# Performance work log

Measured on AMD Instinct MI355X. Metric: run time of the kernel, lower is better.

Reference implementation:

```python
import jax, jax.numpy as jnp
import numpy as np

N, F, K, O = 8192, 512, 2, 64
FMIN = jnp.finfo(jnp.float32).min


def setup_inputs() -> dict:
    key = jax.random.key(0)
    k1, k2, k3, k4, k5 = jax.random.split(key, 5)
    H = jax.random.normal(k1, (N, F), dtype=jnp.float32)
    # sparse-ish binary adjacency with self-loops (float mask, as in TF code)
    A = (jax.random.uniform(k2, (N, N)) < 0.0125).astype(jnp.float32)
    A = jnp.maximum(A, jnp.eye(N, dtype=jnp.float32))
    idx = jnp.arange(N, dtype=jnp.int32)
    W = jax.random.normal(k3, (K, F, O), dtype=jnp.float32) * 0.1
    b = jnp.zeros((K, O), dtype=jnp.float32)
    a1 = jax.random.normal(k4, (K, O), dtype=jnp.float32) * 0.1
    a2 = jax.random.normal(k5, (K, O), dtype=jnp.float32) * 0.1
    return {"H": H, "A": A, "idx": idx, "W": W, "b": b, "a1": a1, "a2": a2}


def reference(H, A, idx, W, b, a1, a2):
    # batch_A = tf.gather(A, idx, axis=1)
    batch_A = A[:, idx]                                  # [N, N]
    HW = jnp.einsum('nf,kfo->kno', H, W)                 # [K, N, O]
    attn1 = jnp.einsum('kno,ko->kn', HW, a1)             # [K, N]
    attn2 = jnp.einsum('kno,ko->kn', HW, a2)             # [K, N]
    # transpose(meshgrid sum): scores[k, i, j] = attn1[k, i] + attn2[k, j]
    scores = attn1[:, :, None] + attn2[:, None, :]       # [K, N, N]
    scores = scores + FMIN * (1.0 - batch_A)[None]
    scores = jnp.where(scores >= 0, scores, 0.2 * scores)  # LeakyReLU(0.2)
    attn = jax.nn.softmax(scores, axis=-1)               # [K, N, N]
    # res = transpose(HW^T @ attn) => res[k, i] = sum_j attn[k, j, i] * HW[k, j]
    res = jnp.einsum('kji,kjo->kio', attn, HW)           # [K, N, O]
    out = jax.nn.relu(res + b[:, None, :])               # [K, N, O]
    # concat heads along feature axis
    return jnp.transpose(out, (1, 0, 2)).reshape(N, K * O)
```

## Files before the change

### kernel.cpp

```cpp
#include <hip/hip_runtime.h>

#define NN 8192
#define FD 512
typedef unsigned long long u64;

__device__ __forceinline__ unsigned f2bf(float x) {
  unsigned u = __float_as_uint(x);
  u += 0x7FFFu + ((u >> 16) & 1u);
  return u >> 16;
}

__device__ __forceinline__ int flt2key(float f) {
  int i = __float_as_int(f);
  return i >= 0 ? i : (i ^ 0x7FFFFFFF);
}
__device__ __forceinline__ float key2flt(int k) {
  return __int_as_float(k >= 0 ? k : (k ^ 0x7FFFFFFF));
}

__device__ __forceinline__ int col0_of_word(int w) {
  return ((w >> 5) << 11) + (((w >> 2) & 7) << 8) + (w & 3);
}

__global__ __launch_bounds__(256) void k1_hw(
    const float* __restrict__ H, const float* __restrict__ W,
    const float* __restrict__ a1, const float* __restrict__ a2,
    const int* __restrict__ idx, int* __restrict__ flag,
    unsigned short* __restrict__ hw2, float* __restrict__ c1, float* __restrict__ c2p,
    int* __restrict__ gkey) {
  if (blockIdx.x >= 512) {
    const int t = (blockIdx.x - 512) * 256 + threadIdx.x;
    int4 v = ((const int4*)idx)[t];
    const int base = t * 4;
    bool bad = (v.x != base) | (v.y != base + 1) | (v.z != base + 2) | (v.w != base + 3);
    const bool any = (__ballot(bad) != 0ULL);
    if ((threadIdx.x & 63) == 0) atomicMax(flag, any ? 1 : 0);
    return;
  }
  const int k    = blockIdx.x & 1;
  const int wv   = threadIdx.x >> 6;
  const int lane = threadIdx.x & 63;
  const int nbase = __builtin_amdgcn_readfirstlane((blockIdx.x >> 1) * 32 + wv * 8);
  const float* __restrict__ Wk = W + k * (FD * 64);
  float acc[8] = {0.f,0.f,0.f,0.f,0.f,0.f,0.f,0.f};
  for (int f = 0; f < FD; f += 4) {
    float w0 = Wk[(f+0)*64 + lane];
    float w1 = Wk[(f+1)*64 + lane];
    float w2 = Wk[(f+2)*64 + lane];
    float w3 = Wk[(f+3)*64 + lane];
#pragma unroll
    for (int r = 0; r < 8; ++r) {
      float4 h = *(const float4*)(H + (size_t)(nbase + r) * FD + f);
      acc[r] = fmaf(h.x, w0, acc[r]);
      acc[r] = fmaf(h.y, w1, acc[r]);
      acc[r] = fmaf(h.z, w2, acc[r]);
      acc[r] = fmaf(h.w, w3, acc[r]);
    }
  }
  const float a1v = a1[k*64 + lane];
  const float a2v = a2[k*64 + lane];
  float wmax = -3.4e38f;
#pragma unroll
  for (int r = 0; r < 8; ++r) {
    const int n = nbase + r;
    hw2[((size_t)n * 64 + lane) * 2 + k] = (unsigned short)f2bf(acc[r]);
    float t1 = acc[r] * a1v;
    float t2 = acc[r] * a2v;
#pragma unroll
    for (int off = 32; off; off >>= 1) {
      t1 += __shfl_down(t1, off);
      t2 += __shfl_down(t2, off);
    }
    if (lane == 0) {
      c1[k*NN + n] = t1;
      c2p[n*2 + k] = t2;
      wmax = fmaxf(wmax, t2);
    }
  }
  if (lane == 0) atomicMax(&gkey[k], flt2key(wmax));
}

__global__ __launch_bounds__(256) void k2_scan(
    const float* __restrict__ A, const int* __restrict__ idx, const int* __restrict__ flag,
    const int* __restrict__ gkey,
    const float* __restrict__ c1, const float* __restrict__ c2p,
    u64* __restrict__ mask, float4* __restrict__ param2) {
  __shared__ u64 sm[128];
  __shared__ float redl[2][4];
  const int tid = threadIdx.x;
  const int wv = tid >> 6, lane = tid & 63;
  const int j = blockIdx.x;
  const bool fast = (flag[0] == 0);
  const float* __restrict__ Arow = A + (size_t)j * NN;

  float4 a[8];
  if (fast) {
#pragma unroll
    for (int p = 0; p < 8; ++p)
      a[p] = *(const float4*)(Arow + wv * 2048 + p * 256 + lane * 4);
  } else {
#pragma unroll
    for (int p = 0; p < 8; ++p) {
      const int c0 = wv * 2048 + p * 256 + lane * 4;
      a[p].x = Arow[idx[c0+0]]; a[p].y = Arow[idx[c0+1]];
      a[p].z = Arow[idx[c0+2]]; a[p].w = Arow[idx[c0+3]];
    }
  }
#pragma unroll
  for (int p = 0; p < 8; ++p) {
    const float av[4] = {a[p].x, a[p].y, a[p].z, a[p].w};
#pragma unroll
    for (int c = 0; c < 4; ++c) {
      const u64 bal = __ballot(av[c] != 0.f);
      if (lane == 0) sm[wv * 32 + p * 4 + c] = bal;
    }
  }
  __syncthreads();
  if (tid < 64) {
    ulonglong2 v;
    v.x = sm[tid * 2];
    v.y = sm[tid * 2 + 1];
    *(ulonglong2*)(mask + (size_t)j * 128 + tid * 2) = v;
  }
  const float c10 = c1[j];
  const float c11 = c1[NN + j];
  float M0 = c10 + key2flt(gkey[0]); M0 = (M0 >= 0.f) ? M0 : 0.2f * M0;
  float M1 = c11 + key2flt(gkey[1]); M1 = (M1 >= 0.f) ? M1 : 0.2f * M1;
  float s0 = 0.f, s1 = 0.f;
  if (tid < 128) {
    u64 m = sm[tid];
    const int cb = col0_of_word(tid);
    while (m) {
      const int b = __builtin_ctzll(m);
      m &= m - 1;
      const float2 cv = *(const float2*)(c2p + (cb + 4 * b) * 2);
      float v0 = c10 + cv.x; v0 = (v0 >= 0.f) ? v0 : 0.2f * v0;
      s0 += __expf(v0 - M0);
      float v1 = c11 + cv.y; v1 = (v1 >= 0.f) ? v1 : 0.2f * v1;
      s1 += __expf(v1 - M1);
    }
  }
#pragma unroll
  for (int off = 32; off; off >>= 1) {
    s0 += __shfl_down(s0, off);
    s1 += __shfl_down(s1, off);
  }
  if (lane == 0) { redl[0][wv] = s0; redl[1][wv] = s1; }
  __syncthreads();
  if (tid == 0) {
    float S0 = redl[0][0] + redl[0][1] + redl[0][2] + redl[0][3];
    float S1 = redl[1][0] + redl[1][1] + redl[1][2] + redl[1][3];
    const float I0 = (S0 > 0.f) ? 1.f / S0 : 0.f;
    const float I1 = (S1 > 0.f) ? 1.f / S1 : 0.f;
    param2[j*2 + 0] = make_float4(c10, (S0 > 0.f) ? M0 : 0.f, I0, 0.f);
    param2[j*2 + 1] = make_float4(c11, (S1 > 0.f) ? M1 : 0.f, I1, 0.f);
  }
}

__device__ __forceinline__ u64 xpose64(u64 x, int lane) {
  const u64 M[6] = {0x00000000FFFFFFFFULL, 0x0000FFFF0000FFFFULL,
                    0x00FF00FF00FF00FFULL, 0x0F0F0F0F0F0F0F0FULL,
                    0x3333333333333333ULL, 0x5555555555555555ULL};
  int d = 32;
#pragma unroll
  for (int s = 0; s < 6; ++s, d >>= 1) {
    u64 y = __shfl_xor(x, d);
    const u64 ML = M[s], MH = ~ML;
    if ((lane & d) == 0) x = (x & ML) | ((y & ML) << d);
    else                 x = (x & MH) | ((y & MH) >> d);
  }
  return x;
}

__global__ __launch_bounds__(256) void kT(
    const u64* __restrict__ mask, unsigned short* __restrict__ edges16,
    int* __restrict__ ecnt4) {
  __shared__ unsigned short seg[4][33][64];
  __shared__ int scnt[4][64];
  const int wv = threadIdx.x >> 6, lane = threadIdx.x & 63;
  const int w  = blockIdx.x;
  const int qq = blockIdx.y;
  const int jst = qq * 2048 + wv * 512;
  int cnt = 0;
#pragma unroll 1
  for (int jt = 0; jt < 8; jt += 4) {
    u64 x[4];
#pragma unroll
    for (int t = 0; t < 4; ++t)
      x[t] = mask[(size_t)(jst + (jt + t) * 64 + lane) * 128 + w];
#pragma unroll
    for (int t = 0; t < 4; ++t) x[t] = xpose64(x[t], lane);
#pragma unroll
    for (int t = 0; t < 4; ++t) {
      u64 m = x[t];
      const int jb = jst + (jt + t) * 64;
      while (m) {
        const int r = __builtin_ctzll(m);
        m &= m - 1;
        if (cnt < 32) seg[wv][cnt][lane] = (unsigned short)(jb + r);
        ++cnt;
      }
    }
  }
  scnt[wv][lane] = min(cnt, 32);
  __syncthreads();
  for (int rr = 0; rr < 16; ++rr) {
    const int r = wv * 16 + rr;
    const int i = col0_of_word(w) + 4 * r;
    const int c0 = scnt[0][r], c1 = scnt[1][r], c2 = scnt[2][r], c3 = scnt[3][r];
    const int o1 = c0, o2 = o1 + c1, o3 = o2 + c2;
    const int tot = min(o3 + c3, 64);
    const int pos = lane;
    if (pos < tot) {
      int s, off;
      if (pos < o1)      { s = 0; off = pos; }
      else if (pos < o2) { s = 1; off = pos - o1; }
      else if (pos < o3) { s = 2; off = pos - o2; }
      else               { s = 3; off = pos - o3; }
      edges16[(size_t)i * 256 + qq * 64 + pos] = seg[s][off][r];
    }
    if (lane == 0) ecnt4[i * 4 + qq] = tot;
  }
}

__global__ __launch_bounds__(256) void k3_aggregate(
    const int* __restrict__ ecnt4, const unsigned short* __restrict__ edges16,
    const float4* __restrict__ param2, const float* __restrict__ c2p,
    const unsigned* __restrict__ hw2, const float* __restrict__ b,
    float* __restrict__ out) {
  __shared__ unsigned short ebuf[4][256];
  const int wv = threadIdx.x >> 6, lane = threadIdx.x & 63;
  const int i = __builtin_amdgcn_readfirstlane(blockIdx.x * 4 + wv);
  const float c20 = c2p[i*2];
  const float c21 = c2p[i*2 + 1];
  const int4 ec = *(const int4*)(ecnt4 + i * 4);
  const unsigned short* __restrict__ e16 = edges16 + (size_t)i * 256;
  int off = 0;
  {
    if (lane < ec.x) ebuf[wv][off + lane] = e16[lane];            off += ec.x;
    if (lane < ec.y) ebuf[wv][off + lane] = e16[64 + lane];       off += ec.y;
    if (lane < ec.z) ebuf[wv][off + lane] = e16[128 + lane];      off += ec.z;
    if (lane < ec.w) ebuf[wv][off + lane] = e16[192 + lane];      off += ec.w;
  }
  __syncthreads();
  const int cnt = off;
  float acc0 = 0.f, acc1 = 0.f;
  int t = 0;
  for (; t + 8 <= cnt; t += 8) {
    const ushort4 j1 = *(const ushort4*)(&ebuf[wv][t]);
    const ushort4 j2 = *(const ushort4*)(&ebuf[wv][t + 4]);
    const int jj[8] = {j1.x, j1.y, j1.z, j1.w, j2.x, j2.y, j2.z, j2.w};
    float4 p0[8], p1[8];
    unsigned uu[8];
#pragma unroll
    for (int s = 0; s < 8; ++s) {
      p0[s] = param2[jj[s]*2];
      p1[s] = param2[jj[s]*2 + 1];
      uu[s] = hw2[(size_t)jj[s] * 64 + lane];
    }
#pragma unroll
    for (int s = 0; s < 8; ++s) {
      float v, w;
      v = p0[s].x + c20; v = (v >= 0.f) ? v : 0.2f*v; w = __expf(v - p0[s].y) * p0[s].z;
      acc0 = fmaf(w, __uint_as_float(uu[s] << 16), acc0);
      v = p1[s].x + c21; v = (v >= 0.f) ? v : 0.2f*v; w = __expf(v - p1[s].y) * p1[s].z;
      acc1 = fmaf(w, __uint_as_float(uu[s] & 0xFFFF0000u), acc1);
    }
  }
  for (; t < cnt; ++t) {
    const int j = ebuf[wv][t];
    const float4 p0 = param2[j*2], p1 = param2[j*2+1];
    const unsigned u = hw2[(size_t)j * 64 + lane];
    float v0 = p0.x + c20; v0 = (v0 >= 0.f) ? v0 : 0.2f*v0;
    float w0 = __expf(v0 - p0.y) * p0.z;
    float v1 = p1.x + c21; v1 = (v1 >= 0.f) ? v1 : 0.2f*v1;
    float w1 = __expf(v1 - p1.y) * p1.z;
    acc0 = fmaf(w0, __uint_as_float(u << 16), acc0);
    acc1 = fmaf(w1, __uint_as_float(u & 0xFFFF0000u), acc1);
  }
  out[(size_t)i * 128 + lane]      = fmaxf(acc0 + b[lane], 0.f);
  out[(size_t)i * 128 + 64 + lane] = fmaxf(acc1 + b[64 + lane], 0.f);
}

extern "C" void kernel_launch(void* const* d_in, const int* in_sizes, int n_in,
                              void* d_out, int out_size, void* d_ws, size_t ws_size,
                              hipStream_t stream) {
  const float* H   = (const float*)d_in[0];
  const float* A   = (const float*)d_in[1];
  const int*   idx = (const int*)d_in[2];
  const float* W   = (const float*)d_in[3];
  const float* b   = (const float*)d_in[4];
  const float* a1  = (const float*)d_in[5];
  const float* a2  = (const float*)d_in[6];
  float* out = (float*)d_out;

  char* ws = (char*)d_ws;
  unsigned short* hw2     = (unsigned short*)(ws + 0);
  float*          c1      = (float*)(ws + 2097152);
  float*          c2p     = (float*)(ws + 2162688);
  float4*         param2  = (float4*)(ws + 2228224);
  int*            flag    = (int*)(ws + 2490368);
  int*            gkey    = (int*)(ws + 2490372);
  u64*            mask    = (u64*)(ws + 2490624);
  unsigned short* edges16 = (unsigned short*)(ws + 10879232);
  int*            ecnt4   = (int*)(ws + 15073536);

  k1_hw<<<520, 256, 0, stream>>>(H, W, a1, a2, idx, flag, hw2, c1, c2p, gkey);
  k2_scan<<<NN, 256, 0, stream>>>(A, idx, flag, gkey, c1, c2p, mask, param2);
  kT<<<dim3(128, 4), 256, 0, stream>>>(mask, edges16, ecnt4);
  k3_aggregate<<<NN / 4, 256, 0, stream>>>(ecnt4, edges16, param2, c2p, (const unsigned*)hw2, b, out);
}
```

Baseline: 536.2 us.

## Fuse scan, transpose and aggregate kernels into one cooperative persistent kernel

Replaces the three separate launches (row scan of A, mask transpose, aggregation) with one cooperative kernel of 512 blocks. Each block loops over 16 rows in the scan phase, then does the transpose and aggregation work, with grid-wide syncs between phases. This removes launch gaps and tail effects between kernels. In exchange it adds grid barrier overhead and lowers parallelism in the A scan, which streams 256MB from memory with only 512 blocks; occupancy is limited by launch_bounds(256,2) and the larger combined shared memory.

After: 696.6 us. 1.3x slower.

```diff
diff --git a/kernel.cpp b/kernel.cpp
--- a/kernel.cpp
+++ b/kernel.cpp
@@ -1,4 +1,7 @@
 #include <hip/hip_runtime.h>
+#include <hip/hip_cooperative_groups.h>
+
+namespace cg = cooperative_groups;
 
 #define NN 8192
 #define FD 512
@@ -80,83 +83,6 @@
   if (lane == 0) atomicMax(&gkey[k], flt2key(wmax));
 }
 
-__global__ __launch_bounds__(256) void k2_scan(
-    const float* __restrict__ A, const int* __restrict__ idx, const int* __restrict__ flag,
-    const int* __restrict__ gkey,
-    const float* __restrict__ c1, const float* __restrict__ c2p,
-    u64* __restrict__ mask, float4* __restrict__ param2) {
-  __shared__ u64 sm[128];
-  __shared__ float redl[2][4];
-  const int tid = threadIdx.x;
-  const int wv = tid >> 6, lane = tid & 63;
-  const int j = blockIdx.x;
-  const bool fast = (flag[0] == 0);
-  const float* __restrict__ Arow = A + (size_t)j * NN;
-
-  float4 a[8];
-  if (fast) {
-#pragma unroll
-    for (int p = 0; p < 8; ++p)
-      a[p] = *(const float4*)(Arow + wv * 2048 + p * 256 + lane * 4);
-  } else {
-#pragma unroll
-    for (int p = 0; p < 8; ++p) {
-      const int c0 = wv * 2048 + p * 256 + lane * 4;
-      a[p].x = Arow[idx[c0+0]]; a[p].y = Arow[idx[c0+1]];
-      a[p].z = Arow[idx[c0+2]]; a[p].w = Arow[idx[c0+3]];
-    }
-  }
-#pragma unroll
-  for (int p = 0; p < 8; ++p) {
-    const float av[4] = {a[p].x, a[p].y, a[p].z, a[p].w};
-#pragma unroll
-    for (int c = 0; c < 4; ++c) {
-      const u64 bal = __ballot(av[c] != 0.f);
-      if (lane == 0) sm[wv * 32 + p * 4 + c] = bal;
-    }
-  }
-  __syncthreads();
-  if (tid < 64) {
-    ulonglong2 v;
-    v.x = sm[tid * 2];
-    v.y = sm[tid * 2 + 1];
-    *(ulonglong2*)(mask + (size_t)j * 128 + tid * 2) = v;
-  }
-  const float c10 = c1[j];
-  const float c11 = c1[NN + j];
-  float M0 = c10 + key2flt(gkey[0]); M0 = (M0 >= 0.f) ? M0 : 0.2f * M0;
-  float M1 = c11 + key2flt(gkey[1]); M1 = (M1 >= 0.f) ? M1 : 0.2f * M1;
-  float s0 = 0.f, s1 = 0.f;
-  if (tid < 128) {
-    u64 m = sm[tid];
-    const int cb = col0_of_word(tid);
-    while (m) {
-      const int b = __builtin_ctzll(m);
-      m &= m - 1;
-      const float2 cv = *(const float2*)(c2p + (cb + 4 * b) * 2);
-      float v0 = c10 + cv.x; v0 = (v0 >= 0.f) ? v0 : 0.2f * v0;
-      s0 += __expf(v0 - M0);
-      float v1 = c11 + cv.y; v1 = (v1 >= 0.f) ? v1 : 0.2f * v1;
-      s1 += __expf(v1 - M1);
-    }
-  }
-#pragma unroll
-  for (int off = 32; off; off >>= 1) {
-    s0 += __shfl_down(s0, off);
-    s1 += __shfl_down(s1, off);
-  }
-  if (lane == 0) { redl[0][wv] = s0; redl[1][wv] = s1; }
-  __syncthreads();
-  if (tid == 0) {
-    float S0 = redl[0][0] + redl[0][1] + redl[0][2] + redl[0][3];
-    float S1 = redl[1][0] + redl[1][1] + redl[1][2] + redl[1][3];
-    const float I0 = (S0 > 0.f) ? 1.f / S0 : 0.f;
-    const float I1 = (S1 > 0.f) ? 1.f / S1 : 0.f;
-    param2[j*2 + 0] = make_float4(c10, (S0 > 0.f) ? M0 : 0.f, I0, 0.f);
-    param2[j*2 + 1] = make_float4(c11, (S1 > 0.f) ? M1 : 0.f, I1, 0.f);
-  }
-}
-
 __device__ __forceinline__ u64 xpose64(u64 x, int lane) {
   const u64 M[6] = {0x00000000FFFFFFFFULL, 0x0000FFFF0000FFFFULL,
                     0x00FF00FF00FF00FFULL, 0x0F0F0F0F0F0F0F0FULL,
@@ -172,114 +98,198 @@
   return x;
 }
 
-__global__ __launch_bounds__(256) void kT(
-    const u64* __restrict__ mask, unsigned short* __restrict__ edges16,
-    int* __restrict__ ecnt4) {
+__global__ __launch_bounds__(256, 2) void mega(
+    const float* __restrict__ A, const int* __restrict__ idx,
+    const int* __restrict__ flag, const int* __restrict__ gkey,
+    const float* __restrict__ c1, const float* __restrict__ c2p,
+    u64* __restrict__ mask, float4* __restrict__ param2,
+    unsigned short* __restrict__ edges16, int* __restrict__ ecnt4,
+    const unsigned* __restrict__ hw2, const float* __restrict__ b,
+    float* __restrict__ out) {
+  cg::grid_group grid = cg::this_grid();
+  __shared__ u64 sm[128];
+  __shared__ float redl[2][4];
   __shared__ unsigned short seg[4][33][64];
   __shared__ int scnt[4][64];
-  const int wv = threadIdx.x >> 6, lane = threadIdx.x & 63;
-  const int w  = blockIdx.x;
-  const int qq = blockIdx.y;
-  const int jst = qq * 2048 + wv * 512;
-  int cnt = 0;
+  __shared__ unsigned short ebuf[4][256];
+
+  const int tid = threadIdx.x;
+  const int wv = tid >> 6, lane = tid & 63;
+
+  {
+    const bool fast = (flag[0] == 0);
+    const float G0 = key2flt(gkey[0]);
+    const float G1 = key2flt(gkey[1]);
 #pragma unroll 1
-  for (int jt = 0; jt < 8; jt += 4) {
-    u64 x[4];
-#pragma unroll
-    for (int t = 0; t < 4; ++t)
-      x[t] = mask[(size_t)(jst + (jt + t) * 64 + lane) * 128 + w];
-#pragma unroll
-    for (int t = 0; t < 4; ++t) x[t] = xpose64(x[t], lane);
-#pragma unroll
-    for (int t = 0; t < 4; ++t) {
-      u64 m = x[t];
-      const int jb = jst + (jt + t) * 64;
-      while (m) {
-        const int r = __builtin_ctzll(m);
-        m &= m - 1;
-        if (cnt < 32) seg[wv][cnt][lane] = (unsigned short)(jb + r);
-        ++cnt;
-      }
-    }
-  }
-  scnt[wv][lane] = min(cnt, 32);
-  __syncthreads();
-  for (int rr = 0; rr < 16; ++rr) {
-    const int r = wv * 16 + rr;
-    const int i = col0_of_word(w) + 4 * r;
-    const int c0 = scnt[0][r], c1 = scnt[1][r], c2 = scnt[2][r], c3 = scnt[3][r];
-    const int o1 = c0, o2 = o1 + c1, o3 = o2 + c2;
-    const int tot = min(o3 + c3, 64);
-    const int pos = lane;
-    if (pos < tot) {
-      int s, off;
-      if (pos < o1)      { s = 0; off = pos; }
-      else if (pos < o2) { s = 1; off = pos - o1; }
-      else if (pos < o3) { s = 2; off = pos - o2; }
-      else               { s = 3; off = pos - o3; }
-      edges16[(size_t)i * 256 + qq * 64 + pos] = seg[s][off][r];
-    }
-    if (lane == 0) ecnt4[i * 4 + qq] = tot;
-  }
-}
-
-__global__ __launch_bounds__(256) void k3_aggregate(
-    const int* __restrict__ ecnt4, const unsigned short* __restrict__ edges16,
-    const float4* __restrict__ param2, const float* __restrict__ c2p,
-    const unsigned* __restrict__ hw2, const float* __restrict__ b,
-    float* __restrict__ out) {
-  __shared__ unsigned short ebuf[4][256];
-  const int wv = threadIdx.x >> 6, lane = threadIdx.x & 63;
-  const int i = __builtin_amdgcn_readfirstlane(blockIdx.x * 4 + wv);
-  const float c20 = c2p[i*2];
-  const float c21 = c2p[i*2 + 1];
-  const int4 ec = *(const int4*)(ecnt4 + i * 4);
-  const unsigned short* __restrict__ e16 = edges16 + (size_t)i * 256;
-  int off = 0;
+    for (int r = 0; r < 16; ++r) {
+      const int j = blockIdx.x * 16 + r;
+      const float* __restrict__ Arow = A + (size_t)j * NN;
+      float4 a[8];
+      if (fast) {
+#pragma unroll
+        for (int p = 0; p < 8; ++p)
+          a[p] = *(const float4*)(Arow + wv * 2048 + p * 256 + lane * 4);
+      } else {
+#pragma unroll
+        for (int p = 0; p < 8; ++p) {
+          const int c0 = wv * 2048 + p * 256 + lane * 4;
+          a[p].x = Arow[idx[c0+0]]; a[p].y = Arow[idx[c0+1]];
+          a[p].z = Arow[idx[c0+2]]; a[p].w = Arow[idx[c0+3]];
+        }
+      }
+#pragma unroll
+      for (int p = 0; p < 8; ++p) {
+        const float av[4] = {a[p].x, a[p].y, a[p].z, a[p].w};
+#pragma unroll
+        for (int c = 0; c < 4; ++c) {
+          const u64 bal = __ballot(av[c] != 0.f);
+          if (lane == 0) sm[wv * 32 + p * 4 + c] = bal;
+        }
+      }
+      __syncthreads();
+      if (tid < 64) {
+        ulonglong2 v;
+        v.x = sm[tid * 2];
+        v.y = sm[tid * 2 + 1];
+        *(ulonglong2*)(mask + (size_t)j * 128 + tid * 2) = v;
+      }
+      const float c10 = c1[j];
+      const float c11 = c1[NN + j];
+      float M0 = c10 + G0; M0 = (M0 >= 0.f) ? M0 : 0.2f * M0;
+      float M1 = c11 + G1; M1 = (M1 >= 0.f) ? M1 : 0.2f * M1;
+      float s0 = 0.f, s1 = 0.f;
+      if (tid < 128) {
+        u64 m = sm[tid];
+        const int cb = col0_of_word(tid);
+        while (m) {
+          const int bb = __builtin_ctzll(m);
+          m &= m - 1;
+          const float2 cv = *(const float2*)(c2p + (cb + 4 * bb) * 2);
+          float v0 = c10 + cv.x; v0 = (v0 >= 0.f) ? v0 : 0.2f * v0;
+          s0 += __expf(v0 - M0);
+          float v1 = c11 + cv.y; v1 = (v1 >= 0.f) ? v1 : 0.2f * v1;
+          s1 += __expf(v1 - M1);
+        }
+      }
+#pragma unroll
+      for (int off = 32; off; off >>= 1) {
+        s0 += __shfl_down(s0, off);
+        s1 += __shfl_down(s1, off);
+      }
+      if (lane == 0) { redl[0][wv] = s0; redl[1][wv] = s1; }
+      __syncthreads();
+      if (tid == 0) {
+        float S0 = redl[0][0] + redl[0][1] + redl[0][2] + redl[0][3];
+        float S1 = redl[1][0] + redl[1][1] + redl[1][2] + redl[1][3];
+        const float I0 = (S0 > 0.f) ? 1.f / S0 : 0.f;
+        const float I1 = (S1 > 0.f) ? 1.f / S1 : 0.f;
+        param2[j*2 + 0] = make_float4(c10, (S0 > 0.f) ? M0 : 0.f, I0, 0.f);
+        param2[j*2 + 1] = make_float4(c11, (S1 > 0.f) ? M1 : 0.f, I1, 0.f);
+      }
+      __syncthreads();
+    }
+  }
+  grid.sync();
+
   {
-    if (lane < ec.x) ebuf[wv][off + lane] = e16[lane];            off += ec.x;
-    if (lane < ec.y) ebuf[wv][off + lane] = e16[64 + lane];       off += ec.y;
-    if (lane < ec.z) ebuf[wv][off + lane] = e16[128 + lane];      off += ec.z;
-    if (lane < ec.w) ebuf[wv][off + lane] = e16[192 + lane];      off += ec.w;
-  }
-  __syncthreads();
-  const int cnt = off;
-  float acc0 = 0.f, acc1 = 0.f;
-  int t = 0;
-  for (; t + 8 <= cnt; t += 8) {
-    const ushort4 j1 = *(const ushort4*)(&ebuf[wv][t]);
-    const ushort4 j2 = *(const ushort4*)(&ebuf[wv][t + 4]);
-    const int jj[8] = {j1.x, j1.y, j1.z, j1.w, j2.x, j2.y, j2.z, j2.w};
-    float4 p0[8], p1[8];
-    unsigned uu[8];
-#pragma unroll
-    for (int s = 0; s < 8; ++s) {
-      p0[s] = param2[jj[s]*2];
-      p1[s] = param2[jj[s]*2 + 1];
-      uu[s] = hw2[(size_t)jj[s] * 64 + lane];
-    }
-#pragma unroll
-    for (int s = 0; s < 8; ++s) {
-      float v, w;
-      v = p0[s].x + c20; v = (v >= 0.f) ? v : 0.2f*v; w = __expf(v - p0[s].y) * p0[s].z;
-      acc0 = fmaf(w, __uint_as_float(uu[s] << 16), acc0);
-      v = p1[s].x + c21; v = (v >= 0.f) ? v : 0.2f*v; w = __expf(v - p1[s].y) * p1[s].z;
-      acc1 = fmaf(w, __uint_as_float(uu[s] & 0xFFFF0000u), acc1);
-    }
-  }
-  for (; t < cnt; ++t) {
-    const int j = ebuf[wv][t];
-    const float4 p0 = param2[j*2], p1 = param2[j*2+1];
-    const unsigned u = hw2[(size_t)j * 64 + lane];
-    float v0 = p0.x + c20; v0 = (v0 >= 0.f) ? v0 : 0.2f*v0;
-    float w0 = __expf(v0 - p0.y) * p0.z;
-    float v1 = p1.x + c21; v1 = (v1 >= 0.f) ? v1 : 0.2f*v1;
-    float w1 = __expf(v1 - p1.y) * p1.z;
-    acc0 = fmaf(w0, __uint_as_float(u << 16), acc0);
-    acc1 = fmaf(w1, __uint_as_float(u & 0xFFFF0000u), acc1);
-  }
-  out[(size_t)i * 128 + lane]      = fmaxf(acc0 + b[lane], 0.f);
-  out[(size_t)i * 128 + 64 + lane] = fmaxf(acc1 + b[64 + lane], 0.f);
+    const int w  = blockIdx.x & 127;
+    const int qq = blockIdx.x >> 7;
+    const int jst = qq * 2048 + wv * 512;
+    int cnt = 0;
+#pragma unroll 1
+    for (int jt = 0; jt < 8; jt += 4) {
+      u64 x[4];
+#pragma unroll
+      for (int t = 0; t < 4; ++t)
+        x[t] = mask[(size_t)(jst + (jt + t) * 64 + lane) * 128 + w];
+#pragma unroll
+      for (int t = 0; t < 4; ++t) x[t] = xpose64(x[t], lane);
+#pragma unroll
+      for (int t = 0; t < 4; ++t) {
+        u64 m = x[t];
+        const int jb = jst + (jt + t) * 64;
+        while (m) {
+          const int r = __builtin_ctzll(m);
+          m &= m - 1;
+          if (cnt < 32) seg[wv][cnt][lane] = (unsigned short)(jb + r);
+          ++cnt;
+        }
+      }
+    }
+    scnt[wv][lane] = min(cnt, 32);
+    __syncthreads();
+    for (int rr = 0; rr < 16; ++rr) {
+      const int r = wv * 16 + rr;
+      const int i = col0_of_word(w) + 4 * r;
+      const int c0 = scnt[0][r], cc1 = scnt[1][r], cc2 = scnt[2][r], cc3 = scnt[3][r];
+      const int o1 = c0, o2 = o1 + cc1, o3 = o2 + cc2;
+      const int tot = min(o3 + cc3, 64);
+      const int pos = lane;
+      if (pos < tot) {
+        int s, off;
+        if (pos < o1)      { s = 0; off = pos; }
+        else if (pos < o2) { s = 1; off = pos - o1; }
+        else if (pos < o3) { s = 2; off = pos - o2; }
+        else               { s = 3; off = pos - o3; }
+        edges16[(size_t)i * 256 + qq * 64 + pos] = seg[s][off][r];
+      }
+      if (lane == 0) ecnt4[i * 4 + qq] = tot;
+    }
+  }
+  grid.sync();
+
+#pragma unroll 1
+  for (int rr = 0; rr < 4; ++rr) {
+    const int i = __builtin_amdgcn_readfirstlane(rr * 2048 + blockIdx.x * 4 + wv);
+    const float c20 = c2p[i*2];
+    const float c21 = c2p[i*2 + 1];
+    const int4 ec = *(const int4*)(ecnt4 + i * 4);
+    const unsigned short* __restrict__ e16 = edges16 + (size_t)i * 256;
+    int off = 0;
+    {
+      if (lane < ec.x) ebuf[wv][off + lane] = e16[lane];            off += ec.x;
+      if (lane < ec.y) ebuf[wv][off + lane] = e16[64 + lane];       off += ec.y;
+      if (lane < ec.z) ebuf[wv][off + lane] = e16[128 + lane];      off += ec.z;
+      if (lane < ec.w) ebuf[wv][off + lane] = e16[192 + lane];      off += ec.w;
+    }
+    const int cnt = off;
+    float acc0 = 0.f, acc1 = 0.f;
+    int t = 0;
+    for (; t + 8 <= cnt; t += 8) {
+      const ushort4 j1 = *(const ushort4*)(&ebuf[wv][t]);
+      const ushort4 j2 = *(const ushort4*)(&ebuf[wv][t + 4]);
+      const int jj[8] = {j1.x, j1.y, j1.z, j1.w, j2.x, j2.y, j2.z, j2.w};
+      float4 p0[8], p1[8];
+      unsigned uu[8];
+#pragma unroll
+      for (int s = 0; s < 8; ++s) {
+        p0[s] = param2[jj[s]*2];
+        p1[s] = param2[jj[s]*2 + 1];
+        uu[s] = hw2[(size_t)jj[s] * 64 + lane];
+      }
+#pragma unroll
+      for (int s = 0; s < 8; ++s) {
+        float v, w;
+        v = p0[s].x + c20; v = (v >= 0.f) ? v : 0.2f*v; w = __expf(v - p0[s].y) * p0[s].z;
+        acc0 = fmaf(w, __uint_as_float(uu[s] << 16), acc0);
+        v = p1[s].x + c21; v = (v >= 0.f) ? v : 0.2f*v; w = __expf(v - p1[s].y) * p1[s].z;
+        acc1 = fmaf(w, __uint_as_float(uu[s] & 0xFFFF0000u), acc1);
+      }
+    }
+    for (; t < cnt; ++t) {
+      const int j = ebuf[wv][t];
+      const float4 p0 = param2[j*2], p1 = param2[j*2+1];
+      const unsigned u = hw2[(size_t)j * 64 + lane];
+      float v0 = p0.x + c20; v0 = (v0 >= 0.f) ? v0 : 0.2f*v0;
+      float w0 = __expf(v0 - p0.y) * p0.z;
+      float v1 = p1.x + c21; v1 = (v1 >= 0.f) ? v1 : 0.2f*v1;
+      float w1 = __expf(v1 - p1.y) * p1.z;
+      acc0 = fmaf(w0, __uint_as_float(u << 16), acc0);
+      acc1 = fmaf(w1, __uint_as_float(u & 0xFFFF0000u), acc1);
+    }
+    out[(size_t)i * 128 + lane]      = fmaxf(acc0 + b[lane], 0.f);
+    out[(size_t)i * 128 + 64 + lane] = fmaxf(acc1 + b[64 + lane], 0.f);
+  }
 }
 
 extern "C" void kernel_launch(void* const* d_in, const int* in_sizes, int n_in,
@@ -306,7 +316,14 @@
   int*            ecnt4   = (int*)(ws + 15073536);
 
   k1_hw<<<520, 256, 0, stream>>>(H, W, a1, a2, idx, flag, hw2, c1, c2p, gkey);
-  k2_scan<<<NN, 256, 0, stream>>>(A, idx, flag, gkey, c1, c2p, mask, param2);
-  kT<<<dim3(128, 4), 256, 0, stream>>>(mask, edges16, ecnt4);
-  k3_aggregate<<<NN / 4, 256, 0, stream>>>(ecnt4, edges16, param2, c2p, (const unsigned*)hw2, b, out);
-}
+
+  const unsigned* hw2u = (const unsigned*)hw2;
+  const int* flagc = flag;
+  const int* gkeyc = gkey;
+  void* args[] = {
+    (void*)&A, (void*)&idx, (void*)&flagc, (void*)&gkeyc,
+    (void*)&c1, (void*)&c2p, (void*)&mask, (void*)&param2,
+    (void*)&edges16, (void*)&ecnt4, (void*)&hw2u, (void*)&b, (void*)&out
+  };
+  hipLaunchCooperativeKernel((const void*)mega, dim3(512), dim3(256), args, 0, stream);
+}
```
